# Kernel tuning notes

Measured on AMD Instinct MI355X. Metric: run time of the kernel, lower is better.

## Reference

```python
import jax, jax.numpy as jnp
import numpy as np

N, E, D, H, L = 50000, 400000, 128, 4, 3
IN_DIM, OUT_DIM = 128, 64
NEG_SLOPE = 0.01
LN_EPS = 1e-5


def setup_inputs() -> dict:
    key = jax.random.key(0)
    ks = jax.random.split(key, 18)
    s = 0.05
    return {
        "x": jax.random.normal(ks[0], (N, IN_DIM), jnp.float32),
        "edge_index": jax.random.randint(ks[1], (2, E), 0, N, jnp.int32),
        "K": jax.random.normal(ks[2], (N,), jnp.float32),
        # input projection
        "W_in": jax.random.normal(ks[3], (IN_DIM, D), jnp.float32) * s,
        "b_in": jnp.zeros((D,), jnp.float32),
        # per-layer params, stacked over L layers
        "Wk_w": jax.random.normal(ks[4], (L, D), jnp.float32) * s,   # Linear(1, dim) weight
        "Wk_b": jnp.zeros((L, D), jnp.float32),
        "Wq": jax.random.normal(ks[5], (L, D, D * H), jnp.float32) * s,
        "Wv": jax.random.normal(ks[6], (L, D, D * H), jnp.float32) * s,
        "att": jax.random.normal(ks[7], (L, H, 3 * D), jnp.float32) * s,  # self.a
        "Wo": jax.random.normal(ks[8], (L, D * H, D), jnp.float32) * s,
        "b_l": jnp.zeros((L, D), jnp.float32),                       # self.b
        "ln_g": jnp.ones((L, D), jnp.float32),
        "ln_b": jnp.zeros((L, D), jnp.float32),
        "gate_w": jax.random.normal(ks[9], (L, D, D), jnp.float32) * s,
        "gate_b": jnp.zeros((L, D), jnp.float32),
        # output projection
        "W_out": jax.random.normal(ks[10], (D, OUT_DIM), jnp.float32) * s,
        "b_out": jnp.zeros((OUT_DIM,), jnp.float32),
    }


def _layer(x, K, src, dst, wkw, wkb, wq, wv, att, wo, bl, lng, lnb, gw, gb):
    # ku: Linear(1, dim) applied to K[:, None]  -> [N, D]
    ku = K[:, None] * wkw[None, :] + wkb
    q = x @ wq  # [N, H*D]
    v = x @ wv  # [N, H*D]
    qi = q[dst].reshape(-1, H, D)   # gather at target i
    vj = v[src].reshape(-1, H, D)   # gather at source j
    kui = ku[dst]                   # [E, D], broadcast over heads
    # (a * cat([ku, qi, vj], -1)).sum(-1) split into three dot products
    a_k, a_q, a_v = att[:, :D], att[:, D:2 * D], att[:, 2 * D:]
    score = (jnp.einsum('ed,hd->eh', kui, a_k)
             + jnp.einsum('ehd,hd->eh', qi, a_q)
             + jnp.einsum('ehd,hd->eh', vj, a_v))  # [E, H]
    e = jnp.where(score > 0, score, NEG_SLOPE * score)  # leaky_relu
    # segment softmax over target index
    mx = jax.ops.segment_max(e, dst, num_segments=N)
    ex = jnp.exp(e - mx[dst])
    sm = jax.ops.segment_sum(ex, dst, num_segments=N)
    alpha = ex / sm[dst]  # [E, H]
    msg = (alpha[:, :, None] * vj).reshape(-1, H * D)
    agg = jax.ops.segment_sum(msg, dst, num_segments=N)  # aggr='add'
    out = agg @ wo + x  # W(out) + residual
    mu = jnp.mean(out, axis=-1, keepdims=True)
    var = jnp.mean((out - mu) ** 2, axis=-1, keepdims=True)
    out = (out - mu) * jax.lax.rsqrt(var + LN_EPS) * lng + lnb
    g = jax.nn.sigmoid(ku @ gw + gb)
    return jax.nn.relu(out * (1.0 + g) + bl)


def reference(x, edge_index, K, W_in, b_in, Wk_w, Wk_b, Wq, Wv, att, Wo, b_l,
              ln_g, ln_b, gate_w, gate_b, W_out, b_out):
    src, dst = edge_index[0], edge_index[1]
    h = jax.nn.relu(x @ W_in + b_in)
    for i in range(L):  # dropout is identity in eval mode
        h = _layer(h, K, src, dst, Wk_w[i], Wk_b[i], Wq[i], Wv[i], att[i],
                   Wo[i], b_l[i], ln_g[i], ln_b[i], gate_w[i], gate_b[i])
    return h @ W_out + b_out
```

## Files before the change

kernel.cpp:

```cpp
#include <hip/hip_runtime.h>

constexpr int NN = 50000;
constexpr int EE = 400000;
constexpr int DD = 128;
constexpr int HH = 4;
constexpr int LL = 3;
constexpr int QV = DD * HH;
constexpr float NEG_SLOPE = 0.01f;
constexpr float LN_EPS = 1e-5f;

static inline int cdiv(int a, int b) { return (a + b - 1) / b; }

#define DEVINL __device__ __forceinline__

typedef __attribute__((ext_vector_type(8))) short bf16x8;
typedef __attribute__((ext_vector_type(8))) unsigned short u16x8;
typedef __attribute__((ext_vector_type(4))) float f32x4;

DEVINL float wave_sum(float v) {
#pragma unroll
  for (int off = 32; off; off >>= 1) v += __shfl_xor(v, off, 64);
  return v;
}

DEVINL float bf2f(unsigned short u) {
  unsigned int t = ((unsigned int)u) << 16;
  float f;
  __builtin_memcpy(&f, &t, 4);
  return f;
}
DEVINL unsigned short f2bf(float f) {
  unsigned int u;
  __builtin_memcpy(&u, &f, 4);
  u = u + 0x7fffu + ((u >> 16) & 1u);
  return (unsigned short)(u >> 16);
}

DEVINL u16x8 pack2f4(float4 f0, float4 f1) {
  u16x8 val;
  val[0] = f2bf(f0.x); val[1] = f2bf(f0.y); val[2] = f2bf(f0.z); val[3] = f2bf(f0.w);
  val[4] = f2bf(f1.x); val[5] = f2bf(f1.y); val[6] = f2bf(f1.z); val[7] = f2bf(f1.w);
  return val;
}

template <typename TA, typename TC, int EPI, int BN>
__global__ __launch_bounds__(256) void gemm64(
    const TA* __restrict__ A, const unsigned short* __restrict__ Bt,
    const float* __restrict__ bias, TC* __restrict__ C, int M, int N, int K) {
  constexpr int BM = 64, BK = 64, PAD = 4;
  constexpr int NF = BN / 16;
  __shared__ unsigned short As[BM][BK + PAD];
  __shared__ unsigned short Bs[BN][BK + PAD];
  const int tid = threadIdx.x;
  const int wave = tid >> 6, lane = tid & 63;
  const int l15 = lane & 15, l4 = lane >> 4;
  const int brow = blockIdx.y * BM, bcol = blockIdx.x * BN;
  const int wr = wave * 16;

  const int arow = tid >> 2, acol = (tid & 3) * 16;
  const int gr = brow + arow;
  const bool aok = (gr < M);
  constexpr int BRS = (BN == 128) ? 1 : 2;
  const int brw = (BN == 128) ? (tid >> 1) : (tid >> 2);
  const int bcl = (BN == 128) ? (tid & 1) * 32 : (tid & 3) * 16;
  constexpr int BNV = (BN == 128) ? 4 : 2;

  u16x8 ra[2], rb[4];

  auto loadA = [&](int k0) {
    if constexpr (sizeof(TA) == 2) {
      const unsigned short* p = (const unsigned short*)A + (size_t)gr * K + k0 + acol;
      ra[0] = aok ? *(const u16x8*)p : u16x8{};
      ra[1] = aok ? *(const u16x8*)(p + 8) : u16x8{};
    } else {
      const float* p = (const float*)A + (size_t)gr * K + k0 + acol;
      if (aok) {
        ra[0] = pack2f4(*(const float4*)p, *(const float4*)(p + 4));
        ra[1] = pack2f4(*(const float4*)(p + 8), *(const float4*)(p + 12));
      } else {
        ra[0] = u16x8{};
        ra[1] = u16x8{};
      }
    }
  };
  auto loadB = [&](int k0) {
    const unsigned short* p = Bt + (size_t)(bcol + brw) * K + k0 + bcl;
#pragma unroll
    for (int j = 0; j < BNV; j++) rb[j] = *(const u16x8*)(p + j * 8);
  };

  f32x4 acc[NF] = {};
  loadA(0);
  loadB(0);

  for (int k0 = 0; k0 < K; k0 += BK) {
    *(u16x8*)&As[arow][acol] = ra[0];
    *(u16x8*)&As[arow][acol + 8] = ra[1];
#pragma unroll
    for (int j = 0; j < BNV; j++) *(u16x8*)&Bs[brw][bcl + j * 8] = rb[j];
    __syncthreads();
    if (k0 + BK < K) {
      loadA(k0 + BK);
      loadB(k0 + BK);
    }
#pragma unroll
    for (int kk = 0; kk < 2; kk++) {
      bf16x8 a = *(const bf16x8*)&As[wr + l15][kk * 32 + l4 * 8];
      bf16x8 b[NF];
#pragma unroll
      for (int n = 0; n < NF; n++) b[n] = *(const bf16x8*)&Bs[n * 16 + l15][kk * 32 + l4 * 8];
#pragma unroll
      for (int n = 0; n < NF; n++)
        acc[n] = __builtin_amdgcn_mfma_f32_16x16x32_bf16(a, b[n], acc[n], 0, 0, 0);
    }
    __syncthreads();
  }

#pragma unroll
  for (int n = 0; n < NF; n++) {
    const int cc = bcol + n * 16 + l15;
#pragma unroll
    for (int j = 0; j < 4; j++) {
      const int rr = brow + wr + l4 * 4 + j;
      if (rr >= M) continue;
      float val = acc[n][j];
      if (bias) val += bias[cc];
      if constexpr (EPI == 1) val = fmaxf(val, 0.f);
      if constexpr (sizeof(TC) == 2)
        C[(size_t)rr * N + cc] = f2bf(val);
      else
        C[(size_t)rr * N + cc] = val;
    }
  }
}

__global__ __launch_bounds__(256) void gemm_wvo(
    const float* __restrict__ Wv_l, const unsigned short* __restrict__ Wot_l,
    unsigned short* __restrict__ WvoT) {
  constexpr int BK = 128, PAD = 4;
  __shared__ unsigned short As[64][BK + PAD];
  const int tid = threadIdx.x;
  const int wave = tid >> 6, lane = tid & 63;
  const int l15 = lane & 15, l4 = lane >> 4;
  const int brow = blockIdx.y * 64;
  const int hh = brow >> 7;
  const int wr = wave * 16;

  f32x4 acc[8] = {};
  {
    const int row = tid >> 2, col0 = (tid & 3) * 32;
    const int i = (brow + row) & 127;
    const float* srow = Wv_l + (size_t)i * QV + hh * DD + col0;
#pragma unroll
    for (int j = 0; j < 4; j++) {
      *(u16x8*)&As[row][col0 + j * 8] =
          pack2f4(*(const float4*)(srow + j * 8), *(const float4*)(srow + j * 8 + 4));
    }
  }
  __syncthreads();
#pragma unroll
  for (int kk = 0; kk < 4; kk++) {
    bf16x8 a = *(const bf16x8*)&As[wr + l15][kk * 32 + l4 * 8];
    bf16x8 b[8];
#pragma unroll
    for (int n = 0; n < 8; n++)
      b[n] = *(const bf16x8*)(Wot_l + (size_t)(n * 16 + l15) * QV + hh * DD + kk * 32 + l4 * 8);
#pragma unroll
    for (int n = 0; n < 8; n++)
      acc[n] = __builtin_amdgcn_mfma_f32_16x16x32_bf16(a, b[n], acc[n], 0, 0, 0);
  }
#pragma unroll
  for (int n = 0; n < 8; n++) {
    const int cc = n * 16 + l15;
#pragma unroll
    for (int j = 0; j < 4; j++) {
      const int rr = brow + wr + l4 * 4 + j;
      WvoT[(size_t)cc * 512 + rr] = f2bf(acc[n][j]);
    }
  }
}

__global__ __launch_bounds__(256) void gemm_wo_ln(
    const unsigned short* __restrict__ Aagg, const unsigned short* __restrict__ Bt,
    const float* __restrict__ Kf, const float* __restrict__ gv,
    const float* __restrict__ lng, const float* __restrict__ lnb,
    const float* __restrict__ bl, unsigned short* __restrict__ h, int M) {
  constexpr int BM = 64, BK = 64, PAD = 4, K = 512, N = 128;
  __shared__ unsigned short As[BM][BK + PAD];
  __shared__ unsigned short Bs[N][BK + PAD];
  const int tid = threadIdx.x;
  const int wave = tid >> 6, lane = tid & 63;
  const int l15 = lane & 15, l4 = lane >> 4;
  const int brow = blockIdx.y * BM;
  const int wr = wave * 16;

  const int arow = tid >> 2, acol = (tid & 3) * 16;
  const int gr = brow + arow;
  const bool aok = (gr < M);
  const int brw = tid >> 1, bcl = (tid & 1) * 32;

  u16x8 ra[2], rb[4];
  auto loadA = [&](int k0) {
    const unsigned short* p = Aagg + (size_t)gr * K + k0 + acol;
    ra[0] = aok ? *(const u16x8*)p : u16x8{};
    ra[1] = aok ? *(const u16x8*)(p + 8) : u16x8{};
  };
  auto loadB = [&](int k0) {
    const unsigned short* p = Bt + (size_t)brw * K + k0 + bcl;
#pragma unroll
    for (int j = 0; j < 4; j++) rb[j] = *(const u16x8*)(p + j * 8);
  };

  f32x4 acc[8] = {};
  loadA(0);
  loadB(0);

  for (int k0 = 0; k0 < K; k0 += BK) {
    *(u16x8*)&As[arow][acol] = ra[0];
    *(u16x8*)&As[arow][acol + 8] = ra[1];
#pragma unroll
    for (int j = 0; j < 4; j++) *(u16x8*)&Bs[brw][bcl + j * 8] = rb[j];
    __syncthreads();
    if (k0 + BK < K) {
      loadA(k0 + BK);
      loadB(k0 + BK);
    }
#pragma unroll
    for (int kk = 0; kk < 2; kk++) {
      bf16x8 a = *(const bf16x8*)&As[wr + l15][kk * 32 + l4 * 8];
      bf16x8 b[8];
#pragma unroll
      for (int n = 0; n < 8; n++) b[n] = *(const bf16x8*)&Bs[n * 16 + l15][kk * 32 + l4 * 8];
#pragma unroll
      for (int n = 0; n < 8; n++)
        acc[n] = __builtin_amdgcn_mfma_f32_16x16x32_bf16(a, b[n], acc[n], 0, 0, 0);
    }
    __syncthreads();
  }

#pragma unroll
  for (int j = 0; j < 4; j++) {
    const int rr = brow + wr + l4 * 4 + j;
    const bool ok = (rr < M);
    float s = 0.f, q = 0.f;
#pragma unroll
    for (int n = 0; n < 8; n++) {
      const int cc = n * 16 + l15;
      float val = acc[n][j] + (ok ? bf2f(h[(size_t)rr * N + cc]) : 0.f);
      acc[n][j] = val;
      s += val;
      q += val * val;
    }
#pragma unroll
    for (int off = 1; off < 16; off <<= 1) {
      s += __shfl_xor(s, off, 64);
      q += __shfl_xor(q, off, 64);
    }
    const float mean = s * (1.f / 128.f);
    const float var = q * (1.f / 128.f) - mean * mean;
    const float rs = rsqrtf(var + LN_EPS);
    const float kn = ok ? Kf[rr] : 0.f;
#pragma unroll
    for (int n = 0; n < 8; n++) {
      const int cc = n * 16 + l15;
      const float y = (acc[n][j] - mean) * rs * lng[cc] + lnb[cc];
      const float g = 1.f / (1.f + __expf(-(kn * gv[cc] + gv[128 + cc])));
      if (ok) h[(size_t)rr * N + cc] = f2bf(fmaxf(y * (1.f + g) + bl[cc], 0.f));
    }
  }
}

__global__ void transp_all(const float* __restrict__ W_in, const float* __restrict__ W_out,
                           const float* __restrict__ Wo,
                           unsigned short* __restrict__ Wint, unsigned short* __restrict__ Woutt,
                           unsigned short* __restrict__ Wot) {
  int idx = blockIdx.x * 256 + threadIdx.x;
  if (idx < 16384) {
    int n = idx >> 7, k = idx & 127;
    Wint[idx] = f2bf(W_in[k * 128 + n]);
    return;
  }
  idx -= 16384;
  if (idx < 8192) {
    int n = idx >> 7, k = idx & 127;
    Woutt[idx] = f2bf(W_out[k * 64 + n]);
    return;
  }
  idx -= 8192;
  if (idx < 3 * 65536) {
    int l = idx >> 16, r = idx & 65535;
    int n = r >> 9, k = r & 511;
    Wot[idx] = f2bf(Wo[l * 65536 + k * 128 + n]);
  }
}

__global__ void zero_int(int* __restrict__ p, int n) {
  int i = blockIdx.x * blockDim.x + threadIdx.x;
  if (i < n) p[i] = 0;
}

__global__ void histo_kernel(const int* __restrict__ dst, int* __restrict__ deg, int E) {
  int e = blockIdx.x * blockDim.x + threadIdx.x;
  if (e < E) atomicAdd(&deg[dst[e]], 1);
}

__global__ __launch_bounds__(1024) void scan_blocks(
    const int* __restrict__ deg, int* __restrict__ rowptr, int* __restrict__ blocksum, int N) {
  __shared__ int lds[1024];
  const int tid = threadIdx.x;
  const int i = blockIdx.x * 1024 + tid;
  int x = (i < N) ? deg[i] : 0;
  lds[tid] = x;
  __syncthreads();
  for (int off = 1; off < 1024; off <<= 1) {
    int t = (tid >= off) ? lds[tid - off] : 0;
    __syncthreads();
    lds[tid] += t;
    __syncthreads();
  }
  if (i < N) rowptr[i] = lds[tid] - x;
  if (tid == 1023) blocksum[blockIdx.x] = lds[1023];
}

__global__ void scan_sums(int* __restrict__ blocksum, int* __restrict__ rowptr, int NB, int N) {
  if (threadIdx.x == 0 && blockIdx.x == 0) {
    int run = 0;
    for (int b = 0; b < NB; b++) {
      int t = blocksum[b];
      blocksum[b] = run;
      run += t;
    }
    rowptr[N] = run;
  }
}

__global__ void scan_apply(int* __restrict__ rowptr, int* __restrict__ cursor,
                           const int* __restrict__ blocksum, int N) {
  int i = blockIdx.x * blockDim.x + threadIdx.x;
  if (i < N) {
    int val = rowptr[i] + blocksum[i >> 10];
    rowptr[i] = val;
    cursor[i] = val;
  }
}

__global__ void scatter_kernel(const int* __restrict__ src, const int* __restrict__ dst,
                               int* __restrict__ cursor, int* __restrict__ esrc,
                               int* __restrict__ edst, int E) {
  int e = blockIdx.x * blockDim.x + threadIdx.x;
  if (e < E) {
    int d = dst[e];
    int pos = atomicAdd(&cursor[d], 1);
    esrc[pos] = src[e];
    edst[pos] = d;
  }
}

__global__ __launch_bounds__(256) void layer_pre(
    const float* __restrict__ wq, const float* __restrict__ wv,
    const float* __restrict__ att_l, const float* __restrict__ wkw,
    const float* __restrict__ wkb, const float* __restrict__ gw,
    const float* __restrict__ gb,
    float* __restrict__ wqv_a, float* __restrict__ kk, float* __restrict__ gv) {
  const int wid = blockIdx.x * 4 + (threadIdx.x >> 6);
  const int lane = threadIdx.x & 63;
  if (wid < 1024) {
    int k = wid >> 3, o = wid & 7;
    const float* w;
    const float* a;
    if (o < 4) {
      w = wq + (size_t)k * QV + o * DD;
      a = att_l + o * 3 * DD + DD;
    } else {
      w = wv + (size_t)k * QV + (o - 4) * DD;
      a = att_l + (o - 4) * 3 * DD + 2 * DD;
    }
    float s = wave_sum(w[lane] * a[lane] + w[lane + 64] * a[lane + 64]);
    if (lane == 0) wqv_a[wid] = s;
  } else if (wid < 1152) {
    int c = wid - 1024;
    float s = wave_sum(wkw[lane] * gw[(size_t)lane * DD + c] +
                       wkw[lane + 64] * gw[(size_t)(lane + 64) * DD + c]);
    if (lane == 0) gv[c] = s;
  } else if (wid < 1280) {
    int c = wid - 1152;
    float s = wave_sum(wkb[lane] * gw[(size_t)lane * DD + c] +
                       wkb[lane + 64] * gw[(size_t)(lane + 64) * DD + c]);
    if (lane == 0) gv[DD + c] = s + gb[c];
  } else if (wid < 1288) {
    int t = wid - 1280;
    const float* a = att_l + (t & 3) * 3 * DD;
    const float* w = (t < 4) ? wkw : wkb;
    float s = wave_sum(w[lane] * a[lane] + w[lane + 64] * a[lane + 64]);
    if (lane == 0) kk[t] = s;
  }
}

__global__ __launch_bounds__(256) void node_pre2(
    const unsigned short* __restrict__ h, const float* __restrict__ Kf,
    const float* __restrict__ wqv_a, const float* __restrict__ kk,
    float* __restrict__ skq, float* __restrict__ svb, int N) {
  __shared__ float W[DD][8];
  __shared__ float kkl[8];
  const int tid = threadIdx.x;
  for (int i = tid; i < DD * 8; i += 256) W[i >> 3][i & 7] = wqv_a[i];
  if (tid < 8) kkl[tid] = kk[tid];
  __syncthreads();
  const int wid = tid >> 6, lane = tid & 63;
  const int n = blockIdx.x * 4 + wid;
  if (n >= N) return;
  const float h0 = bf2f(h[(size_t)n * DD + lane]);
  const float h1 = bf2f(h[(size_t)n * DD + lane + 64]);
  float r[8];
#pragma unroll
  for (int o = 0; o < 8; o++) r[o] = wave_sum(h0 * W[lane][o] + h1 * W[lane + 64][o]);
  if (lane == 0) {
    const float kn = Kf[n];
    *reinterpret_cast<float4*>(skq + (size_t)n * 4) =
        make_float4(r[0] + kn * kkl[0] + kkl[4], r[1] + kn * kkl[1] + kkl[5],
                    r[2] + kn * kkl[2] + kkl[6], r[3] + kn * kkl[3] + kkl[7]);
    *reinterpret_cast<float4*>(svb + (size_t)n * 4) = make_float4(r[4], r[5], r[6], r[7]);
  }
}

__global__ __launch_bounds__(256) void edge_ex(
    const int* __restrict__ esrc, const int* __restrict__ edst,
    const float* __restrict__ skq, const float* __restrict__ svb,
    float4* __restrict__ ext4, int E) {
  const int e = blockIdx.x * 256 + threadIdx.x;
  if (e >= E) return;
  const int s = esrc[e], d = edst[e];
  const float4 sv = *(const float4*)(svb + (size_t)s * 4);
  const float4 kq = *(const float4*)(skq + (size_t)d * 4);
  float sc[4] = {kq.x + sv.x, kq.y + sv.y, kq.z + sv.z, kq.w + sv.w};
  float ex[4];
#pragma unroll
  for (int hh = 0; hh < 4; hh++) {
    float vv = sc[hh] > 0.f ? sc[hh] : NEG_SLOPE * sc[hh];
    ex[hh] = __expf(fminf(vv, 60.f));
  }
  ext4[e] = make_float4(ex[0], ex[1], ex[2], ex[3]);
}

__global__ __launch_bounds__(256) void attn_gather(
    const int* __restrict__ rowptr, const int* __restrict__ esrc,
    const float4* __restrict__ ext4, const unsigned short* __restrict__ h,
    unsigned short* __restrict__ agh, int N) {
  const int wid = threadIdx.x >> 6;
  const int lane = threadIdx.x & 63;
  const int n = blockIdx.x * 4 + wid;
  if (n >= N) return;
  const int beg = rowptr[n];
  const int end = rowptr[n + 1];
  const int c0 = lane * 2;

  float a0[4] = {}, a1[4] = {};
  float sumw[4] = {};

  for (int base = beg; base < end; base += 64) {
    const int cnt = min(64, end - base);
    int myidx = 0;
    if (lane < cnt) myidx = esrc[base + lane];
    int j = 0;
    for (; j + 8 <= cnt; j += 8) {
      int s[8];
      unsigned int wv[8];
      float4 ee[8];
#pragma unroll
      for (int u = 0; u < 8; u++) s[u] = __shfl(myidx, j + u, 64);
#pragma unroll
      for (int u = 0; u < 8; u++) wv[u] = *(const unsigned int*)(h + (size_t)s[u] * DD + c0);
#pragma unroll
      for (int u = 0; u < 8; u++) ee[u] = ext4[base + j + u];
#pragma unroll
      for (int u = 0; u < 8; u++) {
        const float lo = bf2f((unsigned short)(wv[u] & 0xffffu));
        const float hi = bf2f((unsigned short)(wv[u] >> 16));
        a0[0] += ee[u].x * lo; a1[0] += ee[u].x * hi;
        a0[1] += ee[u].y * lo; a1[1] += ee[u].y * hi;
        a0[2] += ee[u].z * lo; a1[2] += ee[u].z * hi;
        a0[3] += ee[u].w * lo; a1[3] += ee[u].w * hi;
        sumw[0] += ee[u].x; sumw[1] += ee[u].y;
        sumw[2] += ee[u].z; sumw[3] += ee[u].w;
      }
    }
    for (; j < cnt; j++) {
      const int s0 = __shfl(myidx, j, 64);
      const unsigned int w0 = *(const unsigned int*)(h + (size_t)s0 * DD + c0);
      const float4 ee = ext4[base + j];
      const float lo = bf2f((unsigned short)(w0 & 0xffffu));
      const float hi = bf2f((unsigned short)(w0 >> 16));
      a0[0] += ee.x * lo; a1[0] += ee.x * hi;
      a0[1] += ee.y * lo; a1[1] += ee.y * hi;
      a0[2] += ee.z * lo; a1[2] += ee.z * hi;
      a0[3] += ee.w * lo; a1[3] += ee.w * hi;
      sumw[0] += ee.x; sumw[1] += ee.y; sumw[2] += ee.z; sumw[3] += ee.w;
    }
  }
  const bool has = (end > beg);
#pragma unroll
  for (int hh = 0; hh < 4; hh++) {
    const float inv = has ? 1.f / sumw[hh] : 0.f;
    const unsigned int packed =
        (unsigned int)f2bf(a0[hh] * inv) | ((unsigned int)f2bf(a1[hh] * inv) << 16);
    *(unsigned int*)(agh + (size_t)n * QV + hh * DD + c0) = packed;
  }
}

extern "C" void kernel_launch(void* const* d_in, const int* in_sizes, int n_in,
                              void* d_out, int out_size, void* d_ws, size_t ws_size,
                              hipStream_t stream) {
  const float* x = (const float*)d_in[0];
  const int* edge = (const int*)d_in[1];
  const float* Kf = (const float*)d_in[2];
  const float* W_in = (const float*)d_in[3];
  const float* b_in = (const float*)d_in[4];
  const float* Wk_w = (const float*)d_in[5];
  const float* Wk_b = (const float*)d_in[6];
  const float* Wq = (const float*)d_in[7];
  const float* Wv = (const float*)d_in[8];
  const float* att = (const float*)d_in[9];
  const float* Wo = (const float*)d_in[10];
  const float* b_l = (const float*)d_in[11];
  const float* ln_g = (const float*)d_in[12];
  const float* ln_b = (const float*)d_in[13];
  const float* gate_w = (const float*)d_in[14];
  const float* gate_b = (const float*)d_in[15];
  const float* W_out = (const float*)d_in[16];
  const float* b_out = (const float*)d_in[17];
  float* out = (float*)d_out;

  const int* src = edge;
  const int* dst = edge + EE;

  char* w = (char*)d_ws;
  auto alloc = [&](size_t bytes) {
    char* p = w;
    w += (bytes + 255) & ~(size_t)255;
    return p;
  };
  unsigned short* h = (unsigned short*)alloc((size_t)NN * DD * 2);
  unsigned short* agh = (unsigned short*)alloc((size_t)NN * QV * 2);
  float* skq = (float*)alloc((size_t)NN * HH * 4);
  float* svb = (float*)alloc((size_t)NN * HH * 4);
  float* wqv_a = (float*)alloc(DD * 8 * 4);
  float* kk = (float*)alloc(8 * 4);
  float* gv = (float*)alloc(2 * DD * 4);
  int* deg = (int*)alloc((size_t)NN * 4);
  int* rowptr = (int*)alloc((size_t)(NN + 1) * 4);
  int* cursor = (int*)alloc((size_t)NN * 4);
  int* esrc = (int*)alloc((size_t)EE * 4);
  int* edst = (int*)alloc((size_t)EE * 4);
  float4* ext4 = (float4*)alloc((size_t)EE * 16);
  int* blocksum = (int*)alloc((size_t)64 * 4);
  unsigned short* Wint = (unsigned short*)alloc((size_t)DD * DD * 2);
  unsigned short* Woutt = (unsigned short*)alloc((size_t)64 * DD * 2);
  unsigned short* Wot = (unsigned short*)alloc((size_t)LL * DD * QV * 2);
  unsigned short* WvoT = (unsigned short*)alloc((size_t)DD * QV * 2);

  dim3 blk(256);
  const int NB = cdiv(NN, 1024);
  const int GY = cdiv(NN, 64);

  zero_int<<<cdiv(NN, 256), blk, 0, stream>>>(deg, NN);
  histo_kernel<<<cdiv(EE, 256), blk, 0, stream>>>(dst, deg, EE);
  scan_blocks<<<NB, 1024, 0, stream>>>(deg, rowptr, blocksum, NN);
  scan_sums<<<1, 64, 0, stream>>>(blocksum, rowptr, NB, NN);
  scan_apply<<<cdiv(NN, 256), blk, 0, stream>>>(rowptr, cursor, blocksum, NN);
  scatter_kernel<<<cdiv(EE, 256), blk, 0, stream>>>(src, dst, cursor, esrc, edst, EE);

  transp_all<<<cdiv(16384 + 8192 + 3 * 65536, 256), blk, 0, stream>>>(
      W_in, W_out, Wo, Wint, Woutt, Wot);

  gemm64<float, unsigned short, 1, 128><<<dim3(1, GY), blk, 0, stream>>>(
      x, Wint, b_in, h, NN, DD, DD);

  for (int l = 0; l < LL; l++) {
    const float* wkw = Wk_w + (size_t)l * DD;
    const float* wkb = Wk_b + (size_t)l * DD;
    const float* wq = Wq + (size_t)l * DD * QV;
    const float* wv = Wv + (size_t)l * DD * QV;
    const float* att_l = att + (size_t)l * HH * 3 * DD;
    const float* bl = b_l + (size_t)l * DD;
    const float* lng = ln_g + (size_t)l * DD;
    const float* lnb = ln_b + (size_t)l * DD;
    const float* gw = gate_w + (size_t)l * DD * DD;
    const float* gb = gate_b + (size_t)l * DD;

    layer_pre<<<cdiv(1288, 4), blk, 0, stream>>>(wq, wv, att_l, wkw, wkb, gw, gb, wqv_a, kk, gv);

    gemm_wvo<<<dim3(1, 8), blk, 0, stream>>>(wv, Wot + (size_t)l * DD * QV, WvoT);

    node_pre2<<<cdiv(NN, 4), blk, 0, stream>>>(h, Kf, wqv_a, kk, skq, svb, NN);

    edge_ex<<<cdiv(EE, 256), blk, 0, stream>>>(esrc, edst, skq, svb, ext4, EE);

    attn_gather<<<cdiv(NN, 4), blk, 0, stream>>>(rowptr, esrc, ext4, h, agh, NN);

    gemm_wo_ln<<<dim3(1, GY), blk, 0, stream>>>(
        agh, WvoT, Kf, gv, lng, lnb, bl, h, NN);
  }

  gemm64<unsigned short, float, 0, 64><<<dim3(1, GY), blk, 0, stream>>>(
      h, Woutt, b_out, out, NN, 64, DD);
}
```

Measured before the change: 540.8 us.

## Fuse attention gather with Wo GEMM and LayerNorm, keep aggregate in shared memory

Merges the per-node attention aggregation kernel into the Wo GEMM plus LayerNorm epilogue. Each block builds a 32-row aggregated tile (512 wide) directly in LDS, so the N×512 bf16 intermediate never goes through global memory. The block tile is halved to 32 rows, with waves split over columns and a cross-wave LDS reduction for the LayerNorm statistics. h is now ping-ponged between two buffers because the gather reads neighbour rows while the epilogue writes the output. The trade-off is larger LDS use (about 50KB), which lowers occupancy, and the gather and GEMM phases no longer overlap across blocks.

```diff
diff --git a/kernel.cpp b/kernel.cpp
--- a/kernel.cpp
+++ b/kernel.cpp
@@ -60,7 +60,6 @@
   const int arow = tid >> 2, acol = (tid & 3) * 16;
   const int gr = brow + arow;
   const bool aok = (gr < M);
-  constexpr int BRS = (BN == 128) ? 1 : 2;
   const int brw = (BN == 128) ? (tid >> 1) : (tid >> 2);
   const int bcl = (BN == 128) ? (tid & 1) * 32 : (tid & 3) * 16;
   constexpr int BNV = (BN == 128) ? 4 : 2;
@@ -180,72 +179,127 @@
   }
 }
 
-__global__ __launch_bounds__(256) void gemm_wo_ln(
-    const unsigned short* __restrict__ Aagg, const unsigned short* __restrict__ Bt,
-    const float* __restrict__ Kf, const float* __restrict__ gv,
-    const float* __restrict__ lng, const float* __restrict__ lnb,
-    const float* __restrict__ bl, unsigned short* __restrict__ h, int M) {
-  constexpr int BM = 64, BK = 64, PAD = 4, K = 512, N = 128;
-  __shared__ unsigned short As[BM][BK + PAD];
+__global__ __launch_bounds__(256) void attn_wo_ln(
+    const int* __restrict__ rowptr, const int* __restrict__ esrc,
+    const float4* __restrict__ ext4, const unsigned short* __restrict__ h,
+    const unsigned short* __restrict__ Bt, const float* __restrict__ Kf,
+    const float* __restrict__ gv, const float* __restrict__ lng,
+    const float* __restrict__ lnb, const float* __restrict__ bl,
+    unsigned short* __restrict__ hnew, int M) {
+  constexpr int BM = 32, BK = 64, PAD = 4, K = 512, N = 128;
+  __shared__ unsigned short Ag[BM][K + PAD];
   __shared__ unsigned short Bs[N][BK + PAD];
+  __shared__ float redS[BM][2], redQ[BM][2];
   const int tid = threadIdx.x;
   const int wave = tid >> 6, lane = tid & 63;
   const int l15 = lane & 15, l4 = lane >> 4;
-  const int brow = blockIdx.y * BM;
-  const int wr = wave * 16;
-
-  const int arow = tid >> 2, acol = (tid & 3) * 16;
-  const int gr = brow + arow;
-  const bool aok = (gr < M);
+  const int brow = blockIdx.x * BM;
+
   const int brw = tid >> 1, bcl = (tid & 1) * 32;
-
-  u16x8 ra[2], rb[4];
-  auto loadA = [&](int k0) {
-    const unsigned short* p = Aagg + (size_t)gr * K + k0 + acol;
-    ra[0] = aok ? *(const u16x8*)p : u16x8{};
-    ra[1] = aok ? *(const u16x8*)(p + 8) : u16x8{};
-  };
+  u16x8 rb[4];
   auto loadB = [&](int k0) {
     const unsigned short* p = Bt + (size_t)brw * K + k0 + bcl;
 #pragma unroll
     for (int j = 0; j < 4; j++) rb[j] = *(const u16x8*)(p + j * 8);
   };
-
-  f32x4 acc[8] = {};
-  loadA(0);
   loadB(0);
 
+  const int c0 = lane * 2;
+  for (int i = 0; i < 8; i++) {
+    const int n = brow + wave * 8 + i;
+    const int nl = wave * 8 + i;
+    if (n < M) {
+      const int beg = rowptr[n];
+      const int end = rowptr[n + 1];
+      float a0[4] = {}, a1[4] = {};
+      float sumw[4] = {};
+      for (int base = beg; base < end; base += 64) {
+        const int cnt = min(64, end - base);
+        int myidx = 0;
+        if (lane < cnt) myidx = esrc[base + lane];
+        int j = 0;
+        for (; j + 8 <= cnt; j += 8) {
+          int s[8];
+          unsigned int wv[8];
+          float4 ee[8];
+#pragma unroll
+          for (int u = 0; u < 8; u++) s[u] = __shfl(myidx, j + u, 64);
+#pragma unroll
+          for (int u = 0; u < 8; u++) wv[u] = *(const unsigned int*)(h + (size_t)s[u] * DD + c0);
+#pragma unroll
+          for (int u = 0; u < 8; u++) ee[u] = ext4[base + j + u];
+#pragma unroll
+          for (int u = 0; u < 8; u++) {
+            const float lo = bf2f((unsigned short)(wv[u] & 0xffffu));
+            const float hi = bf2f((unsigned short)(wv[u] >> 16));
+            a0[0] += ee[u].x * lo; a1[0] += ee[u].x * hi;
+            a0[1] += ee[u].y * lo; a1[1] += ee[u].y * hi;
+            a0[2] += ee[u].z * lo; a1[2] += ee[u].z * hi;
+            a0[3] += ee[u].w * lo; a1[3] += ee[u].w * hi;
+            sumw[0] += ee[u].x; sumw[1] += ee[u].y;
+            sumw[2] += ee[u].z; sumw[3] += ee[u].w;
+          }
+        }
+        for (; j < cnt; j++) {
+          const int s0 = __shfl(myidx, j, 64);
+          const unsigned int w0 = *(const unsigned int*)(h + (size_t)s0 * DD + c0);
+          const float4 ee = ext4[base + j];
+          const float lo = bf2f((unsigned short)(w0 & 0xffffu));
+          const float hi = bf2f((unsigned short)(w0 >> 16));
+          a0[0] += ee.x * lo; a1[0] += ee.x * hi;
+          a0[1] += ee.y * lo; a1[1] += ee.y * hi;
+          a0[2] += ee.z * lo; a1[2] += ee.z * hi;
+          a0[3] += ee.w * lo; a1[3] += ee.w * hi;
+          sumw[0] += ee.x; sumw[1] += ee.y; sumw[2] += ee.z; sumw[3] += ee.w;
+        }
+      }
+      const bool has = (end > beg);
+#pragma unroll
+      for (int hh = 0; hh < 4; hh++) {
+        const float inv = has ? 1.f / sumw[hh] : 0.f;
+        const unsigned int packed =
+            (unsigned int)f2bf(a0[hh] * inv) | ((unsigned int)f2bf(a1[hh] * inv) << 16);
+        *(unsigned int*)&Ag[nl][hh * DD + c0] = packed;
+      }
+    } else {
+#pragma unroll
+      for (int hh = 0; hh < 4; hh++) *(unsigned int*)&Ag[nl][hh * DD + c0] = 0u;
+    }
+  }
+  __syncthreads();
+
+  const int wr = (wave & 1) * 16;
+  const int wc = (wave >> 1) * 64;
+  f32x4 acc[4] = {};
+
   for (int k0 = 0; k0 < K; k0 += BK) {
-    *(u16x8*)&As[arow][acol] = ra[0];
-    *(u16x8*)&As[arow][acol + 8] = ra[1];
 #pragma unroll
     for (int j = 0; j < 4; j++) *(u16x8*)&Bs[brw][bcl + j * 8] = rb[j];
     __syncthreads();
-    if (k0 + BK < K) {
-      loadA(k0 + BK);
-      loadB(k0 + BK);
-    }
+    if (k0 + BK < K) loadB(k0 + BK);
 #pragma unroll
     for (int kk = 0; kk < 2; kk++) {
-      bf16x8 a = *(const bf16x8*)&As[wr + l15][kk * 32 + l4 * 8];
-      bf16x8 b[8];
-#pragma unroll
-      for (int n = 0; n < 8; n++) b[n] = *(const bf16x8*)&Bs[n * 16 + l15][kk * 32 + l4 * 8];
-#pragma unroll
-      for (int n = 0; n < 8; n++)
+      bf16x8 a = *(const bf16x8*)&Ag[wr + l15][k0 + kk * 32 + l4 * 8];
+      bf16x8 b[4];
+#pragma unroll
+      for (int n = 0; n < 4; n++) b[n] = *(const bf16x8*)&Bs[wc + n * 16 + l15][kk * 32 + l4 * 8];
+#pragma unroll
+      for (int n = 0; n < 4; n++)
         acc[n] = __builtin_amdgcn_mfma_f32_16x16x32_bf16(a, b[n], acc[n], 0, 0, 0);
     }
     __syncthreads();
   }
 
+  const int wavecol = wave >> 1;
 #pragma unroll
   for (int j = 0; j < 4; j++) {
-    const int rr = brow + wr + l4 * 4 + j;
+    const int rloc = wr + l4 * 4 + j;
+    const int rr = brow + rloc;
     const bool ok = (rr < M);
     float s = 0.f, q = 0.f;
 #pragma unroll
-    for (int n = 0; n < 8; n++) {
-      const int cc = n * 16 + l15;
+    for (int n = 0; n < 4; n++) {
+      const int cc = wc + n * 16 + l15;
       float val = acc[n][j] + (ok ? bf2f(h[(size_t)rr * N + cc]) : 0.f);
       acc[n][j] = val;
       s += val;
@@ -256,16 +310,29 @@
       s += __shfl_xor(s, off, 64);
       q += __shfl_xor(q, off, 64);
     }
-    const float mean = s * (1.f / 128.f);
-    const float var = q * (1.f / 128.f) - mean * mean;
+    if (l15 == 0) {
+      redS[rloc][wavecol] = s;
+      redQ[rloc][wavecol] = q;
+    }
+  }
+  __syncthreads();
+#pragma unroll
+  for (int j = 0; j < 4; j++) {
+    const int rloc = wr + l4 * 4 + j;
+    const int rr = brow + rloc;
+    if (rr >= M) continue;
+    const float sum = redS[rloc][0] + redS[rloc][1];
+    const float sq = redQ[rloc][0] + redQ[rloc][1];
+    const float mean = sum * (1.f / 128.f);
+    const float var = sq * (1.f / 128.f) - mean * mean;
     const float rs = rsqrtf(var + LN_EPS);
-    const float kn = ok ? Kf[rr] : 0.f;
-#pragma unroll
-    for (int n = 0; n < 8; n++) {
-      const int cc = n * 16 + l15;
+    const float kn = Kf[rr];
+#pragma unroll
+    for (int n = 0; n < 4; n++) {
+      const int cc = wc + n * 16 + l15;
       const float y = (acc[n][j] - mean) * rs * lng[cc] + lnb[cc];
       const float g = 1.f / (1.f + __expf(-(kn * gv[cc] + gv[128 + cc])));
-      if (ok) h[(size_t)rr * N + cc] = f2bf(fmaxf(y * (1.f + g) + bl[cc], 0.f));
+      hnew[(size_t)rr * N + cc] = f2bf(fmaxf(y * (1.f + g) + bl[cc], 0.f));
     }
   }
 }
@@ -440,71 +507,6 @@
     ex[hh] = __expf(fminf(vv, 60.f));
   }
   ext4[e] = make_float4(ex[0], ex[1], ex[2], ex[3]);
-}
-
-__global__ __launch_bounds__(256) void attn_gather(
-    const int* __restrict__ rowptr, const int* __restrict__ esrc,
-    const float4* __restrict__ ext4, const unsigned short* __restrict__ h,
-    unsigned short* __restrict__ agh, int N) {
-  const int wid = threadIdx.x >> 6;
-  const int lane = threadIdx.x & 63;
-  const int n = blockIdx.x * 4 + wid;
-  if (n >= N) return;
-  const int beg = rowptr[n];
-  const int end = rowptr[n + 1];
-  const int c0 = lane * 2;
-
-  float a0[4] = {}, a1[4] = {};
-  float sumw[4] = {};
-
-  for (int base = beg; base < end; base += 64) {
-    const int cnt = min(64, end - base);
-    int myidx = 0;
-    if (lane < cnt) myidx = esrc[base + lane];
-    int j = 0;
-    for (; j + 8 <= cnt; j += 8) {
-      int s[8];
-      unsigned int wv[8];
-      float4 ee[8];
-#pragma unroll
-      for (int u = 0; u < 8; u++) s[u] = __shfl(myidx, j + u, 64);
-#pragma unroll
-      for (int u = 0; u < 8; u++) wv[u] = *(const unsigned int*)(h + (size_t)s[u] * DD + c0);
-#pragma unroll
-      for (int u = 0; u < 8; u++) ee[u] = ext4[base + j + u];
-#pragma unroll
-      for (int u = 0; u < 8; u++) {
-        const float lo = bf2f((unsigned short)(wv[u] & 0xffffu));
-        const float hi = bf2f((unsigned short)(wv[u] >> 16));
-        a0[0] += ee[u].x * lo; a1[0] += ee[u].x * hi;
-        a0[1] += ee[u].y * lo; a1[1] += ee[u].y * hi;
-        a0[2] += ee[u].z * lo; a1[2] += ee[u].z * hi;
-        a0[3] += ee[u].w * lo; a1[3] += ee[u].w * hi;
-        sumw[0] += ee[u].x; sumw[1] += ee[u].y;
-        sumw[2] += ee[u].z; sumw[3] += ee[u].w;
-      }
-    }
-    for (; j < cnt; j++) {
-      const int s0 = __shfl(myidx, j, 64);
-      const unsigned int w0 = *(const unsigned int*)(h + (size_t)s0 * DD + c0);
-      const float4 ee = ext4[base + j];
-      const float lo = bf2f((unsigned short)(w0 & 0xffffu));
-      const float hi = bf2f((unsigned short)(w0 >> 16));
-      a0[0] += ee.x * lo; a1[0] += ee.x * hi;
-      a0[1] += ee.y * lo; a1[1] += ee.y * hi;
-      a0[2] += ee.z * lo; a1[2] += ee.z * hi;
-      a0[3] += ee.w * lo; a1[3] += ee.w * hi;
-      sumw[0] += ee.x; sumw[1] += ee.y; sumw[2] += ee.z; sumw[3] += ee.w;
-    }
-  }
-  const bool has = (end > beg);
-#pragma unroll
-  for (int hh = 0; hh < 4; hh++) {
-    const float inv = has ? 1.f / sumw[hh] : 0.f;
-    const unsigned int packed =
-        (unsigned int)f2bf(a0[hh] * inv) | ((unsigned int)f2bf(a1[hh] * inv) << 16);
-    *(unsigned int*)(agh + (size_t)n * QV + hh * DD + c0) = packed;
-  }
 }
 
 extern "C" void kernel_launch(void* const* d_in, const int* in_sizes, int n_in,
@@ -539,8 +541,8 @@
     w += (bytes + 255) & ~(size_t)255;
     return p;
   };
-  unsigned short* h = (unsigned short*)alloc((size_t)NN * DD * 2);
-  unsigned short* agh = (unsigned short*)alloc((size_t)NN * QV * 2);
+  unsigned short* h0 = (unsigned short*)alloc((size_t)NN * DD * 2);
+  unsigned short* h1 = (unsigned short*)alloc((size_t)NN * DD * 2);
   float* skq = (float*)alloc((size_t)NN * HH * 4);
   float* svb = (float*)alloc((size_t)NN * HH * 4);
   float* wqv_a = (float*)alloc(DD * 8 * 4);
@@ -573,7 +575,10 @@
       W_in, W_out, Wo, Wint, Woutt, Wot);
 
   gemm64<float, unsigned short, 1, 128><<<dim3(1, GY), blk, 0, stream>>>(
-      x, Wint, b_in, h, NN, DD, DD);
+      x, Wint, b_in, h0, NN, DD, DD);
+
+  unsigned short* hcur = h0;
+  unsigned short* hnxt = h1;
 
   for (int l = 0; l < LL; l++) {
     const float* wkw = Wk_w + (size_t)l * DD;
@@ -591,16 +596,16 @@
 
     gemm_wvo<<<dim3(1, 8), blk, 0, stream>>>(wv, Wot + (size_t)l * DD * QV, WvoT);
 
-    node_pre2<<<cdiv(NN, 4), blk, 0, stream>>>(h, Kf, wqv_a, kk, skq, svb, NN);
+    node_pre2<<<cdiv(NN, 4), blk, 0, stream>>>(hcur, Kf, wqv_a, kk, skq, svb, NN);
 
     edge_ex<<<cdiv(EE, 256), blk, 0, stream>>>(esrc, edst, skq, svb, ext4, EE);
 
-    attn_gather<<<cdiv(NN, 4), blk, 0, stream>>>(rowptr, esrc, ext4, h, agh, NN);
-
-    gemm_wo_ln<<<dim3(1, GY), blk, 0, stream>>>(
-        agh, WvoT, Kf, gv, lng, lnb, bl, h, NN);
+    attn_wo_ln<<<cdiv(NN, 32), blk, 0, stream>>>(
+        rowptr, esrc, ext4, hcur, WvoT, Kf, gv, lng, lnb, bl, hnxt, NN);
+
+    unsigned short* t = hcur; hcur = hnxt; hnxt = t;
   }
 
   gemm64<unsigned short, float, 0, 64><<<dim3(1, GY), blk, 0, stream>>>(
-      h, Woutt, b_out, out, NN, 64, DD);
-}
+      hcur, Woutt, b_out, out, NN, 64, DD);
+}
```

After: 614.6 us. 13.6% more time.
